# Kernel tuning notes

Measured on AMD Instinct MI355X. Metric: run time of the kernel, lower is better.

## Reference

```python
import jax, jax.numpy as jnp
import numpy as np

B, N, IN, HD, NH, L, OUT = 256, 128, 9, 128, 8, 4, 60
DH = HD // NH
ALPHA = 0.6
EPS = 1e-5

def _ln(x, g, b):
    m = jnp.mean(x, axis=-1, keepdims=True)
    v = jnp.mean((x - m) ** 2, axis=-1, keepdims=True)
    return (x - m) * jax.lax.rsqrt(v + EPS) * g + b

def setup_inputs():
    key = jax.random.key(0)
    ks = jax.random.split(key, 30)
    p = lambda i, s: jax.random.normal(ks[i], s, jnp.float32) * 0.02
    strong = (jax.random.uniform(ks[25], (N, N)) < 0.15).astype(jnp.float32)
    strong = jnp.maximum(strong, jnp.eye(N, dtype=jnp.float32))  # self loops
    weak_mask = (jax.random.uniform(ks[26], (N, N)) < 0.10).astype(jnp.float32)
    return {
        'x': jax.random.normal(ks[0], (B, N, IN), jnp.float32),
        'conv_w': p(1, (HD, IN)), 'conv_b': p(2, (HD,)),
        'bn_gamma': jnp.ones((HD,), jnp.float32), 'bn_beta': jnp.zeros((HD,), jnp.float32),
        'bn_mean': jnp.zeros((HD,), jnp.float32), 'bn_var': jnp.ones((HD,), jnp.float32),
        'W': p(3, (L, HD, HD)), 'a_src': p(4, (L, NH, DH)), 'a_dst': p(5, (L, NH, DH)),
        'ln_g': jnp.ones((L, HD), jnp.float32), 'ln_b': jnp.zeros((L, HD), jnp.float32),
        'ffn_w1': p(6, (L, HD, 2 * HD)), 'ffn_b1': p(7, (L, 2 * HD)),
        'ffn_w2': p(8, (L, 2 * HD, HD)), 'ffn_b2': p(9, (L, HD)),
        'norm_g': jnp.ones((HD,), jnp.float32), 'norm_b': jnp.zeros((HD,), jnp.float32),
        'proj_w': p(10, (HD, HD)), 'proj_b': p(11, (HD,)),
        'head_w1': p(12, (HD, HD // 2)), 'head_b1': p(13, (HD // 2,)),
        'head_w2': p(14, (HD // 2, OUT)), 'head_b2': p(15, (OUT,)),
        'strong_adj': strong, 'weak_mask': weak_mask,
        'weak_param': p(16, (N, N)), 'edge_weight_adj': p(17, (N, N)),
    }

def reference(x, conv_w, conv_b, bn_gamma, bn_beta, bn_mean, bn_var, W, a_src, a_dst, ln_g, ln_b, ffn_w1, ffn_b1, ffn_w2, ffn_b2, norm_g, norm_b, proj_w, proj_b, head_w1, head_b1, head_w2, head_b2, strong_adj, weak_mask, weak_param, edge_weight_adj):
    # embedding: Conv1d(k=1) == per-node linear, then eval-mode BatchNorm1d + ReLU
    h = jnp.einsum('bni,oi->bno', x, conv_w) + conv_b  # [B,N,HD]
    h = (h - bn_mean) * jax.lax.rsqrt(bn_var + EPS) * bn_gamma + bn_beta
    h = jax.nn.relu(h)
    # weak adjacency: learnable gated edges, row-normalized (shared across layers)
    Aw = jax.nn.sigmoid(weak_param) * weak_mask
    Aw = Aw / (jnp.sum(Aw, axis=-1, keepdims=True) + EPS)  # [N,N]
    for i in range(L):
        res = h
        hp = jnp.einsum('bnd,de->bne', h, W[i]).reshape(B, N, NH, DH)
        s = jnp.einsum('bnhd,hd->bnh', hp, a_src[i])
        t = jnp.einsum('bnhd,hd->bnh', hp, a_dst[i])
        e = jax.nn.leaky_relu(s[:, :, None, :] + t[:, None, :, :], 0.2)  # [B,N,N,H]
        e = e + edge_weight_adj[None, :, :, None]  # learned per-edge bias
        e = jnp.where(strong_adj[None, :, :, None] > 0, e, jnp.float32(-1e9))
        att = jax.nn.softmax(e, axis=2)  # softmax over neighbors j
        strong_out = jnp.einsum('bijh,bjhd->bihd', att, hp)
        weak_out = jnp.einsum('ij,bjhd->bihd', Aw, hp)
        g = jax.nn.relu(ALPHA * strong_out + (1.0 - ALPHA) * weak_out).reshape(B, N, HD)
        g = _ln(g, ln_g[i], ln_b[i])
        g = jax.nn.relu(g @ ffn_w1[i] + ffn_b1[i]) @ ffn_w2[i] + ffn_b2[i]
        h = g + res
    h = _ln(h, norm_g, norm_b)
    h = h @ proj_w + proj_b
    h = jnp.mean(h, axis=1)  # mean-pool over nodes -> [B,HD]
    h = jax.nn.relu(h @ head_w1 + head_b1)
    return h @ head_w2 + head_b2  # [B,OUT]
```

## Files before the change

kernel.cpp:

```cpp
#include <hip/hip_runtime.h>
#include <hip/hip_bf16.h>

typedef __hip_bfloat16 bf16;
typedef unsigned short u16;
typedef __attribute__((ext_vector_type(8))) short bfrag;
typedef __attribute__((ext_vector_type(4))) float cfrag;

union BF { bfrag v; u16 u[8]; unsigned w[4]; };
union CF { cfrag v; float f[4]; };

#define MFMA(a,b,c) __builtin_amdgcn_mfma_f32_16x16x32_bf16(a,b,c,0,0,0)

#define BB   256
#define NN   128
#define IND  9
#define HDD  128
#define LLY  4
#define OUTD 60
#define LOG2E 1.44269504f
#define STR  136

__device__ __forceinline__ float b2f(bf16 v){ return __bfloat162float(v); }
__device__ __forceinline__ float u2f(u16 u){ return __uint_as_float(((unsigned)u) << 16); }
__device__ __forceinline__ u16 f2bf_bits(float f){
    unsigned u = __float_as_uint(f);
    return (u16)((u + 0x7FFFu + ((u >> 16) & 1u)) >> 16);
}
__device__ __forceinline__ unsigned pk2(float a, float b){
    union { __hip_bfloat162 h; unsigned u; } c;
    c.h = __float22bfloat162_rn(make_float2(a, b));
    return c.u;
}
__device__ __forceinline__ float wave_sum(float v){
    #pragma unroll
    for (int m = 32; m; m >>= 1) v += __shfl_xor(v, m, 64);
    return v;
}
__device__ __forceinline__ float ldin(const void* p, int i, bool isbf){
    return isbf ? b2f(((const bf16*)p)[i]) : ((const float*)p)[i];
}

struct SrcPtrs { const void* p[28]; };

__device__ const int NCV_OFF[19] = {0,1152,1280,1408,1536,1664,1792,2304,2816,3840,
                                    4352,4480,4608,20992,21120,29312,29376,33216,33276};
__device__ const int NCV_SRC[18] = {1,2,3,4,5,6,10,11,13,15,16,17,18,19,20,21,22,23};

__global__ __launch_bounds__(256) void k_prep(
    SrcPtrs S, float* __restrict__ pf,
    u16* __restrict__ WT, u16* __restrict__ w1T, u16* __restrict__ w2T,
    u16* __restrict__ WAb, u16* __restrict__ ew2, u16* __restrict__ Aw16,
    int* __restrict__ flagOut)
{
    const unsigned* xw = (const unsigned*)S.p[0];
    int lane = threadIdx.x & 63;
    int cnt = 0;
    for (int i = lane; i < 512; i += 64) {
        float v = __uint_as_float((xw[i] & 0xFFFFu) << 16);
        if (!(fabsf(v) < 32.f)) cnt++;
    }
    bool isbf = wave_sum((float)cnt) < 16.f;
    if (blockIdx.x == 0 && threadIdx.x == 0) *flagOut = isbf ? 1 : 0;

    int blk = blockIdx.x, tid = threadIdx.x;
    if (blk < 131) {
        int idx = blk * 256 + tid;
        if (idx < 33276) {
            int y = 17;
            #pragma unroll 1
            for (int t = 1; t < 18; t++) if (idx < NCV_OFF[t]) { y = t - 1; break; }
            pf[idx] = ldin(S.p[NCV_SRC[y]], idx - NCV_OFF[y], isbf);
        }
    } else if (blk < 387) {
        int j = (blk - 131) * 256 + tid;
        int l = j >> 14, r = j & 16383, n = r >> 7, k = r & 127;
        WT[j] = f2bf_bits(ldin(S.p[7], (l << 14) + k * 128 + n, isbf));
    } else if (blk < 899) {
        int j = (blk - 387) * 256 + tid;
        int l = j >> 15, r = j & 32767, n = r >> 7, k = r & 127;
        w1T[j] = f2bf_bits(ldin(S.p[12], (l << 15) + k * 256 + n, isbf));
    } else if (blk < 1411) {
        int j = (blk - 899) * 256 + tid;
        int l = j >> 15, r = j & 32767, n = r >> 8, k = r & 255;
        w2T[j] = f2bf_bits(ldin(S.p[14], (l << 15) + k * 128 + n, isbf));
    } else if (blk < 1443) {
        int j = (blk - 1411) * 256 + tid;
        int l = j >> 11, r = j & 2047, n = r >> 7, k = r & 127;
        int h = n & 7;
        const void* ap = (n < 8) ? S.p[8] : S.p[9];
        float sacc = 0.f;
        #pragma unroll 1
        for (int d = 0; d < 16; d++)
            sacc += ldin(S.p[7], l * 16384 + k * 128 + h * 16 + d, isbf)
                  * ldin(ap, l * 128 + h * 16 + d, isbf);
        WAb[j] = f2bf_bits(sacc);
    } else if (blk < 1507) {
        int j = (blk - 1443) * 256 + tid;
        float sav = ldin(S.p[24], j, isbf);
        float ewv = ldin(S.p[27], j, isbf);
        ew2[j] = f2bf_bits(sav > 0.f ? ewv * LOG2E : -1e30f);
    } else {
        __shared__ float red[2];
        int i = blk - 1507, j = tid & 127;
        float v = 0.f;
        if (tid < 128) {
            float wmv = ldin(S.p[25], i * 128 + j, isbf);
            float wpv = ldin(S.p[26], i * 128 + j, isbf);
            v = wmv / (1.f + __expf(-wpv));
            float sm = wave_sum(v);
            if ((tid & 63) == 0) red[tid >> 6] = sm;
        }
        __syncthreads();
        if (tid < 128) {
            float tot = red[0] + red[1];
            Aw16[i * 128 + j] = f2bf_bits(v / (tot + 1e-5f));
        }
    }
}

#define LDSB (2*128*STR*2 + 8192)
__global__ __launch_bounds__(512, 2) void k_net(
    const void* __restrict__ xraw, const int* __restrict__ flag,
    const float* __restrict__ pf,
    const u16* __restrict__ WTg, const u16* __restrict__ WAbg,
    const u16* __restrict__ Awg, const u16* __restrict__ ew2g,
    const u16* __restrict__ w1Tg, const u16* __restrict__ w2Tg,
    void* __restrict__ outv)
{
    extern __shared__ __align__(16) char smem[];
    u16* Abuf = (u16*)smem;
    u16* Bbuf = Abuf + 128 * STR;
    float* st2 = (float*)(Bbuf + 128 * STR);
    float* s2  = st2;
    u16*   t2u = (u16*)(st2 + 1024);

    const int b = blockIdx.x;
    const int tid = threadIdx.x, lane = tid & 63, wv = tid >> 6;
    const int l15 = lane & 15, kg = lane >> 4;
    const int wrow = wv * 16;
    const bool isbf = (*flag != 0);

    float hreg[8][4];

    {
        float xr[4][9];
        #pragma unroll
        for (int r = 0; r < 4; r++) {
            int bn = b * NN + wrow + kg * 4 + r;
            #pragma unroll
            for (int k = 0; k < IND; k++) xr[r][k] = ldin(xraw, bn * IND + k, isbf);
        }
        #pragma unroll 1
        for (int nt = 0; nt < 8; nt++) {
            int d = nt * 16 + l15;
            float cwreg[IND];
            #pragma unroll
            for (int k = 0; k < IND; k++) cwreg[k] = pf[d * IND + k];
            float scale = rsqrtf(pf[1664 + d] + 1e-5f) * pf[1280 + d];
            float bias  = pf[1408 + d] - pf[1536 + d] * scale;
            float cbd   = pf[1152 + d];
            #pragma unroll
            for (int r = 0; r < 4; r++) {
                float a = cbd;
                #pragma unroll
                for (int k = 0; k < IND; k++) a = fmaf(xr[r][k], cwreg[k], a);
                a = fmaxf(fmaf(a, scale, bias), 0.f);
                hreg[nt][r] = a;
                Abuf[(wrow + kg * 4 + r) * STR + d] = f2bf_bits(a);
            }
        }
    }

    const int arow = wrow + l15;

    #pragma unroll 1
    for (int l = 0; l < LLY; l++) {
        const u16* WT  = WTg  + l * 16384;
        const u16* WAb = WAbg + l * 2048;
        const u16* w1T = w1Tg + l * 32768;
        const u16* w2T = w2Tg + l * 32768;
        const float* fb1 = pf + 2816 + l * 256;
        const float* fb2 = pf + 3840 + l * 128;
        const float* lng = pf + 1792 + l * 128;
        const float* lnb = pf + 2304 + l * 128;

        __syncthreads();

        {
            CF acc[8], ast;
            #pragma unroll
            for (int r = 0; r < 4; r++) ast.f[r] = 0.f;
            #pragma unroll
            for (int nt = 0; nt < 8; nt++)
                #pragma unroll
                for (int r = 0; r < 4; r++) acc[nt].f[r] = 0.f;
            #pragma unroll 1
            for (int kk = 0; kk < 4; kk++) {
                bfrag af  = *(const bfrag*)&Abuf[arow * STR + kk*32 + kg*8];
                bfrag wab = *(const bfrag*)&WAb[l15 * 128 + kk*32 + kg*8];
                ast.v = MFMA(af, wab, ast.v);
                #pragma unroll
                for (int nt = 0; nt < 8; nt++) {
                    bfrag bw = *(const bfrag*)&WT[(nt*16 + l15) * 128 + kk*32 + kg*8];
                    acc[nt].v = MFMA(af, bw, acc[nt].v);
                }
            }
            #pragma unroll
            for (int nt = 0; nt < 8; nt++) {
                int col = nt*16 + l15;
                #pragma unroll
                for (int rp = 0; rp < 2; rp++) {
                    int row = wrow + kg*4 + rp*2;
                    *(unsigned*)&Bbuf[col * STR + row] = pk2(acc[nt].f[rp*2], acc[nt].f[rp*2+1]);
                }
            }
            #pragma unroll
            for (int r = 0; r < 4; r++) {
                int node = wrow + kg*4 + r;
                float v = ast.f[r] * LOG2E;
                if (l15 < 8) s2[l15 * 128 + node] = v;
                else         t2u[(l15 - 8) * 128 + node] = f2bf_bits(v);
            }
        }
        __syncthreads();

        CF accW[8];
        #pragma unroll
        for (int nt = 0; nt < 8; nt++)
            #pragma unroll
            for (int r = 0; r < 4; r++) accW[nt].f[r] = 0.f;
        #pragma unroll 1
        for (int kk = 0; kk < 4; kk++) {
            bfrag awf = *(const bfrag*)&Awg[arow * 128 + kk*32 + kg*8];
            #pragma unroll
            for (int nt = 0; nt < 8; nt++) {
                bfrag hb2 = *(const bfrag*)&Bbuf[(nt*16 + l15) * STR + kk*32 + kg*8];
                accW[nt].v = MFMA(awf, hb2, accW[nt].v);
            }
        }

        CF accS[8];
        #pragma unroll
        for (int nt = 0; nt < 8; nt++)
            #pragma unroll
            for (int r = 0; r < 4; r++) accS[nt].f[r] = 0.f;
        #pragma unroll 1
        for (int h = 0; h < 8; h++) {
            bfrag hb[4];
            #pragma unroll
            for (int kk = 0; kk < 4; kk++)
                hb[kk] = *(const bfrag*)&Bbuf[(h*16 + l15) * STR + kk*32 + kg*8];
            float sA = s2[h * 128 + arow];
            float pv[4][8];
            float sm = 0.f;
            #pragma unroll
            for (int kk = 0; kk < 4; kk++) {
                BF tb; tb.v = *(const bfrag*)&t2u[h * 128 + kk*32 + kg*8];
                BF e2; e2.v = *(const bfrag*)&ew2g[arow * 128 + kk*32 + kg*8];
                #pragma unroll
                for (int j = 0; j < 8; j++) {
                    float x2 = sA + u2f(tb.u[j]);
                    float lk = fmaxf(x2, 0.2f * x2);
                    float p = __builtin_amdgcn_exp2f(lk + u2f(e2.u[j]));
                    pv[kk][j] = p; sm += p;
                }
            }
            sm += __shfl_xor(sm, 16, 64);
            sm += __shfl_xor(sm, 32, 64);
            float inv = __builtin_amdgcn_rcpf(sm);
            #pragma unroll
            for (int kk = 0; kk < 4; kk++) {
                BF pb;
                #pragma unroll
                for (int q = 0; q < 4; q++)
                    pb.w[q] = pk2(pv[kk][2*q] * inv, pv[kk][2*q+1] * inv);
                accS[h].v = MFMA(pb.v, hb[kk], accS[h].v);
            }
        }
        __syncthreads();

        {
            float gv[8][4];
            #pragma unroll
            for (int nt = 0; nt < 8; nt++)
                #pragma unroll
                for (int r = 0; r < 4; r++)
                    gv[nt][r] = fmaxf(0.6f * accS[nt].f[r] + 0.4f * accW[nt].f[r], 0.f);
            #pragma unroll
            for (int r = 0; r < 4; r++) {
                float s1 = 0.f, sq = 0.f;
                #pragma unroll
                for (int nt = 0; nt < 8; nt++) { float x = gv[nt][r]; s1 += x; sq = fmaf(x, x, sq); }
                #pragma unroll
                for (int m = 1; m <= 8; m <<= 1) { s1 += __shfl_xor(s1, m, 64); sq += __shfl_xor(sq, m, 64); }
                float mu = s1 * (1.f / 128.f);
                float var = sq * (1.f / 128.f) - mu * mu;
                float rs = rsqrtf(fmaxf(var, 0.f) + 1e-5f);
                #pragma unroll
                for (int nt = 0; nt < 8; nt++) {
                    int col = nt*16 + l15;
                    Bbuf[(wrow + kg*4 + r) * STR + col] =
                        f2bf_bits(fmaf((gv[nt][r] - mu) * rs, lng[col], lnb[col]));
                }
            }
        }

        CF acc2[8];
        #pragma unroll
        for (int nt = 0; nt < 8; nt++)
            #pragma unroll
            for (int r = 0; r < 4; r++) acc2[nt].f[r] = 0.f;
        #pragma unroll 1
        for (int nh = 0; nh < 2; nh++) {
            CF a1[8];
            #pragma unroll
            for (int nt = 0; nt < 8; nt++)
                #pragma unroll
                for (int r = 0; r < 4; r++) a1[nt].f[r] = 0.f;
            #pragma unroll 1
            for (int kk = 0; kk < 4; kk++) {
                bfrag gf = *(const bfrag*)&Bbuf[arow * STR + kk*32 + kg*8];
                #pragma unroll
                for (int nt = 0; nt < 8; nt++) {
                    bfrag wf = *(const bfrag*)&w1T[(nh*128 + nt*16 + l15) * 128 + kk*32 + kg*8];
                    a1[nt].v = MFMA(gf, wf, a1[nt].v);
                }
            }
            #pragma unroll
            for (int nt = 0; nt < 8; nt++) {
                int col = nt*16 + l15;
                float b1v = fb1[nh*128 + col];
                #pragma unroll
                for (int r = 0; r < 4; r++)
                    Abuf[(wrow + kg*4 + r) * STR + col] = f2bf_bits(fmaxf(a1[nt].f[r] + b1v, 0.f));
            }
            #pragma unroll 1
            for (int kk = 0; kk < 4; kk++) {
                bfrag hf = *(const bfrag*)&Abuf[arow * STR + kk*32 + kg*8];
                #pragma unroll
                for (int nt = 0; nt < 8; nt++) {
                    bfrag wf = *(const bfrag*)&w2T[(nt*16 + l15) * 256 + nh*128 + kk*32 + kg*8];
                    acc2[nt].v = MFMA(hf, wf, acc2[nt].v);
                }
            }
        }

        #pragma unroll
        for (int nt = 0; nt < 8; nt++) {
            float b2v = fb2[nt*16 + l15];
            #pragma unroll
            for (int r = 0; r < 4; r++) hreg[nt][r] += acc2[nt].f[r] + b2v;
        }
        if (l < LLY - 1) {
            #pragma unroll
            for (int nt = 0; nt < 8; nt++) {
                int col = nt*16 + l15;
                #pragma unroll
                for (int r = 0; r < 4; r++)
                    Abuf[(wrow + kg*4 + r) * STR + col] = f2bf_bits(hreg[nt][r]);
            }
        }
    }

    const float* ng = pf + 4352;
    const float* nb = pf + 4480;
    float pacc[8];
    #pragma unroll
    for (int nt = 0; nt < 8; nt++) pacc[nt] = 0.f;
    #pragma unroll
    for (int r = 0; r < 4; r++) {
        float s1 = 0.f, sq = 0.f;
        #pragma unroll
        for (int nt = 0; nt < 8; nt++) { float x = hreg[nt][r]; s1 += x; sq = fmaf(x, x, sq); }
        #pragma unroll
        for (int m = 1; m <= 8; m <<= 1) { s1 += __shfl_xor(s1, m, 64); sq += __shfl_xor(sq, m, 64); }
        float mu = s1 * (1.f / 128.f);
        float var = sq * (1.f / 128.f) - mu * mu;
        float rs = rsqrtf(fmaxf(var, 0.f) + 1e-5f);
        #pragma unroll
        for (int nt = 0; nt < 8; nt++) {
            int col = nt*16 + l15;
            pacc[nt] += fmaf((hreg[nt][r] - mu) * rs, ng[col], nb[col]);
        }
    }
    #pragma unroll
    for (int nt = 0; nt < 8; nt++) {
        pacc[nt] += __shfl_xor(pacc[nt], 16, 64);
        pacc[nt] += __shfl_xor(pacc[nt], 32, 64);
    }
    __syncthreads();
    if (kg == 0) {
        #pragma unroll
        for (int nt = 0; nt < 8; nt++) st2[wv * 128 + nt*16 + l15] = pacc[nt];
    }
    __syncthreads();
    if (tid < 128) {
        float tot = 0.f;
        #pragma unroll
        for (int w = 0; w < 8; w++) tot += st2[w * 128 + tid];
        st2[1024 + tid] = tot * (1.f / 128.f);
    }
    __syncthreads();
    {
        int e = tid & 127, kq = tid >> 7;
        float a = 0.f;
        #pragma unroll 4
        for (int k = kq * 32; k < kq * 32 + 32; k++)
            a = fmaf(st2[1024 + k], pf[4608 + k * 128 + e], a);
        st2[1152 + kq * 128 + e] = a;
    }
    __syncthreads();
    if (tid < 128)
        st2[1664 + tid] = st2[1152 + tid] + st2[1280 + tid] + st2[1408 + tid] + st2[1536 + tid]
                        + pf[20992 + tid];
    __syncthreads();
    if (tid < 64) {
        float a1 = pf[29312 + tid];
        #pragma unroll 4
        for (int k = 0; k < 128; k++) a1 = fmaf(st2[1664 + k], pf[21120 + k * 64 + tid], a1);
        st2[1792 + tid] = fmaxf(a1, 0.f);
    }
    __syncthreads();
    if (tid < OUTD) {
        float a2 = pf[33216 + tid];
        #pragma unroll 4
        for (int k = 0; k < 64; k++) a2 = fmaf(st2[1792 + k], pf[29376 + k * OUTD + tid], a2);
        if (isbf) ((bf16*)outv)[b * OUTD + tid] = __float2bfloat16(a2);
        else      ((float*)outv)[b * OUTD + tid] = a2;
    }
}

extern "C" void kernel_launch(void* const* d_in, const int* in_sizes, int n_in,
                              void* d_out, int out_size, void* d_ws, size_t ws_size,
                              hipStream_t stream)
{
    float* ws = (float*)d_ws;
    float* pf = ws;
    int*   flag = (int*)(ws + 33280);
    u16* WT16   = (u16*)(ws + 33536);
    u16* w1T16  = WT16 + 65536;
    u16* w2T16  = w1T16 + 131072;
    u16* WAb16  = w2T16 + 131072;
    u16* Aw16   = WAb16 + 8192;
    u16* ew2p   = Aw16 + 16384;

    SrcPtrs S;
    for (int i = 0; i < 28; i++) S.p[i] = d_in[i];

    hipFuncSetAttribute((const void*)k_net,
                        hipFuncAttributeMaxDynamicSharedMemorySize, LDSB);

    k_prep<<<1635, 256, 0, stream>>>(S, pf, WT16, w1T16, w2T16, WAb16, ew2p, Aw16, flag);
    k_net<<<BB, 512, LDSB, stream>>>(d_in[0], flag, pf,
                                     WT16, WAb16, Aw16, ew2p, w1T16, w2T16, d_out);
}
```

Measured before the change: 352.9 us.

## Tile weight transposes in prep and fold weak aggregation into attention accumulator

The prep kernel now transposes weights through a shared-memory tile, which gives coalesced reads and shrinks the grid from 1635 to 435 blocks. In the main kernel, the residual state moves from registers into an fp32 LDS buffer to free registers. Softmax normalisation is deferred: unnormalised probabilities feed the MFMA and are scaled per row afterwards. The weak-adjacency matmul, with 0.4 folded into Aw, accumulates into the same accumulators, and several k-loops are fully unrolled. LDS use grows by about 68KB, which may reduce occupancy below the 2 blocks per CU the launch bounds request.

Result: slower. 401.5 us (+13.8%).

```diff
diff --git a/kernel.cpp b/kernel.cpp
--- a/kernel.cpp
+++ b/kernel.cpp
@@ -52,6 +52,7 @@
     u16* __restrict__ WAb, u16* __restrict__ ew2, u16* __restrict__ Aw16,
     int* __restrict__ flagOut)
 {
+    __shared__ float tile[64][65];
     const unsigned* xw = (const unsigned*)S.p[0];
     int lane = threadIdx.x & 63;
     int cnt = 0;
@@ -71,20 +72,35 @@
             for (int t = 1; t < 18; t++) if (idx < NCV_OFF[t]) { y = t - 1; break; }
             pf[idx] = ldin(S.p[NCV_SRC[y]], idx - NCV_OFF[y], isbf);
         }
-    } else if (blk < 387) {
-        int j = (blk - 131) * 256 + tid;
-        int l = j >> 14, r = j & 16383, n = r >> 7, k = r & 127;
-        WT[j] = f2bf_bits(ldin(S.p[7], (l << 14) + k * 128 + n, isbf));
-    } else if (blk < 899) {
-        int j = (blk - 387) * 256 + tid;
-        int l = j >> 15, r = j & 32767, n = r >> 7, k = r & 127;
-        w1T[j] = f2bf_bits(ldin(S.p[12], (l << 15) + k * 256 + n, isbf));
-    } else if (blk < 1411) {
-        int j = (blk - 899) * 256 + tid;
-        int l = j >> 15, r = j & 32767, n = r >> 8, k = r & 255;
-        w2T[j] = f2bf_bits(ldin(S.p[14], (l << 15) + k * 128 + n, isbf));
-    } else if (blk < 1443) {
-        int j = (blk - 1411) * 256 + tid;
+    } else if (blk < 211) {
+        const void* src; u16* dst; int K, N, k0, n0;
+        if (blk < 147) {
+            int t = blk - 131, l = t >> 2, tt = t & 3;
+            src = (const char*)S.p[7] + (size_t)l * 16384 * (isbf ? 2 : 4);
+            dst = WT + l * 16384; K = 128; N = 128; k0 = (tt >> 1) * 64; n0 = (tt & 1) * 64;
+        } else if (blk < 179) {
+            int t = blk - 147, l = t >> 3, tt = t & 7;
+            src = (const char*)S.p[12] + (size_t)l * 32768 * (isbf ? 2 : 4);
+            dst = w1T + l * 32768; K = 128; N = 256; k0 = (tt >> 2) * 64; n0 = (tt & 3) * 64;
+        } else {
+            int t = blk - 179, l = t >> 3, tt = t & 7;
+            src = (const char*)S.p[14] + (size_t)l * 32768 * (isbf ? 2 : 4);
+            dst = w2T + l * 32768; K = 256; N = 128; k0 = (tt & 3) * 64; n0 = (tt >> 2) * 64;
+        }
+        int ty = tid >> 6, tx = tid & 63;
+        #pragma unroll 4
+        for (int i = 0; i < 16; i++) {
+            int row = ty * 16 + i;
+            tile[row][tx] = ldin(src, (k0 + row) * N + n0 + tx, isbf);
+        }
+        __syncthreads();
+        #pragma unroll 4
+        for (int i = 0; i < 16; i++) {
+            int row = ty * 16 + i;
+            dst[(n0 + row) * K + k0 + tx] = f2bf_bits(tile[tx][row]);
+        }
+    } else if (blk < 243) {
+        int j = (blk - 211) * 256 + tid;
         int l = j >> 11, r = j & 2047, n = r >> 7, k = r & 127;
         int h = n & 7;
         const void* ap = (n < 8) ? S.p[8] : S.p[9];
@@ -94,14 +110,14 @@
             sacc += ldin(S.p[7], l * 16384 + k * 128 + h * 16 + d, isbf)
                   * ldin(ap, l * 128 + h * 16 + d, isbf);
         WAb[j] = f2bf_bits(sacc);
-    } else if (blk < 1507) {
-        int j = (blk - 1443) * 256 + tid;
+    } else if (blk < 307) {
+        int j = (blk - 243) * 256 + tid;
         float sav = ldin(S.p[24], j, isbf);
         float ewv = ldin(S.p[27], j, isbf);
         ew2[j] = f2bf_bits(sav > 0.f ? ewv * LOG2E : -1e30f);
     } else {
         __shared__ float red[2];
-        int i = blk - 1507, j = tid & 127;
+        int i = blk - 307, j = tid & 127;
         float v = 0.f;
         if (tid < 128) {
             float wmv = ldin(S.p[25], i * 128 + j, isbf);
@@ -113,12 +129,12 @@
         __syncthreads();
         if (tid < 128) {
             float tot = red[0] + red[1];
-            Aw16[i * 128 + j] = f2bf_bits(v / (tot + 1e-5f));
-        }
-    }
-}
-
-#define LDSB (2*128*STR*2 + 8192)
+            Aw16[i * 128 + j] = f2bf_bits(0.4f * v / (tot + 1e-5f));
+        }
+    }
+}
+
+#define LDSB (128*STR*2*2 + 128*132*4 + 2560*4)
 __global__ __launch_bounds__(512, 2) void k_net(
     const void* __restrict__ xraw, const int* __restrict__ flag,
     const float* __restrict__ pf,
@@ -128,22 +144,23 @@
     void* __restrict__ outv)
 {
     extern __shared__ __align__(16) char smem[];
-    u16* Abuf = (u16*)smem;
-    u16* Bbuf = Abuf + 128 * STR;
-    float* st2 = (float*)(Bbuf + 128 * STR);
-    float* s2  = st2;
-    u16*   t2u = (u16*)(st2 + 1024);
+    u16* U1 = (u16*)smem;
+    u16* U2 = U1 + 128 * STR;
+    float* hf32 = (float*)(U2 + 128 * STR);
+    float* st2  = hf32 + 128 * 132;
+    float* s2   = st2;
+    u16*   t2u  = (u16*)(st2 + 1024);
+    float* invb = st2 + 1536;
 
     const int b = blockIdx.x;
     const int tid = threadIdx.x, lane = tid & 63, wv = tid >> 6;
     const int l15 = lane & 15, kg = lane >> 4;
     const int wrow = wv * 16;
+    const int arow = wrow + l15;
     const bool isbf = (*flag != 0);
 
-    float hreg[8][4];
-
     {
-        float xr[4][9];
+        float xr[4][IND];
         #pragma unroll
         for (int r = 0; r < 4; r++) {
             int bn = b * NN + wrow + kg * 4 + r;
@@ -165,13 +182,12 @@
                 #pragma unroll
                 for (int k = 0; k < IND; k++) a = fmaf(xr[r][k], cwreg[k], a);
                 a = fmaxf(fmaf(a, scale, bias), 0.f);
-                hreg[nt][r] = a;
-                Abuf[(wrow + kg * 4 + r) * STR + d] = f2bf_bits(a);
-            }
-        }
-    }
-
-    const int arow = wrow + l15;
+                int row = wrow + kg * 4 + r;
+                hf32[row * 132 + d] = a;
+                U1[row * STR + d] = f2bf_bits(a);
+            }
+        }
+    }
 
     #pragma unroll 1
     for (int l = 0; l < LLY; l++) {
@@ -194,9 +210,9 @@
             for (int nt = 0; nt < 8; nt++)
                 #pragma unroll
                 for (int r = 0; r < 4; r++) acc[nt].f[r] = 0.f;
-            #pragma unroll 1
+            #pragma unroll
             for (int kk = 0; kk < 4; kk++) {
-                bfrag af  = *(const bfrag*)&Abuf[arow * STR + kk*32 + kg*8];
+                bfrag af  = *(const bfrag*)&U1[arow * STR + kk*32 + kg*8];
                 bfrag wab = *(const bfrag*)&WAb[l15 * 128 + kk*32 + kg*8];
                 ast.v = MFMA(af, wab, ast.v);
                 #pragma unroll
@@ -211,7 +227,7 @@
                 #pragma unroll
                 for (int rp = 0; rp < 2; rp++) {
                     int row = wrow + kg*4 + rp*2;
-                    *(unsigned*)&Bbuf[col * STR + row] = pk2(acc[nt].f[rp*2], acc[nt].f[rp*2+1]);
+                    *(unsigned*)&U2[col * STR + row] = pk2(acc[nt].f[rp*2], acc[nt].f[rp*2+1]);
                 }
             }
             #pragma unroll
@@ -224,87 +240,79 @@
         }
         __syncthreads();
 
-        CF accW[8];
+        CF accS[8];
         #pragma unroll
         for (int nt = 0; nt < 8; nt++)
             #pragma unroll
-            for (int r = 0; r < 4; r++) accW[nt].f[r] = 0.f;
-        #pragma unroll 1
-        for (int kk = 0; kk < 4; kk++) {
-            bfrag awf = *(const bfrag*)&Awg[arow * 128 + kk*32 + kg*8];
-            #pragma unroll
-            for (int nt = 0; nt < 8; nt++) {
-                bfrag hb2 = *(const bfrag*)&Bbuf[(nt*16 + l15) * STR + kk*32 + kg*8];
-                accW[nt].v = MFMA(awf, hb2, accW[nt].v);
-            }
-        }
-
-        CF accS[8];
-        #pragma unroll
-        for (int nt = 0; nt < 8; nt++)
-            #pragma unroll
             for (int r = 0; r < 4; r++) accS[nt].f[r] = 0.f;
+        BF e2f[4];
+        #pragma unroll
+        for (int kk = 0; kk < 4; kk++)
+            e2f[kk].v = *(const bfrag*)&ew2g[arow * 128 + kk*32 + kg*8];
         #pragma unroll 1
         for (int h = 0; h < 8; h++) {
-            bfrag hb[4];
-            #pragma unroll
-            for (int kk = 0; kk < 4; kk++)
-                hb[kk] = *(const bfrag*)&Bbuf[(h*16 + l15) * STR + kk*32 + kg*8];
             float sA = s2[h * 128 + arow];
-            float pv[4][8];
             float sm = 0.f;
             #pragma unroll
             for (int kk = 0; kk < 4; kk++) {
+                bfrag hb = *(const bfrag*)&U2[(h*16 + l15) * STR + kk*32 + kg*8];
                 BF tb; tb.v = *(const bfrag*)&t2u[h * 128 + kk*32 + kg*8];
-                BF e2; e2.v = *(const bfrag*)&ew2g[arow * 128 + kk*32 + kg*8];
+                BF pb;
+                float p0[8];
                 #pragma unroll
                 for (int j = 0; j < 8; j++) {
                     float x2 = sA + u2f(tb.u[j]);
                     float lk = fmaxf(x2, 0.2f * x2);
-                    float p = __builtin_amdgcn_exp2f(lk + u2f(e2.u[j]));
-                    pv[kk][j] = p; sm += p;
+                    float p = __builtin_amdgcn_exp2f(lk + u2f(e2f[kk].u[j]));
+                    p0[j] = p; sm += p;
                 }
+                #pragma unroll
+                for (int q = 0; q < 4; q++) pb.w[q] = pk2(p0[2*q], p0[2*q+1]);
+                accS[h].v = MFMA(pb.v, hb, accS[h].v);
             }
             sm += __shfl_xor(sm, 16, 64);
             sm += __shfl_xor(sm, 32, 64);
-            float inv = __builtin_amdgcn_rcpf(sm);
-            #pragma unroll
-            for (int kk = 0; kk < 4; kk++) {
-                BF pb;
-                #pragma unroll
-                for (int q = 0; q < 4; q++)
-                    pb.w[q] = pk2(pv[kk][2*q] * inv, pv[kk][2*q+1] * inv);
-                accS[h].v = MFMA(pb.v, hb[kk], accS[h].v);
-            }
-        }
+            invb[h * 128 + arow] = 0.6f * __builtin_amdgcn_rcpf(sm);
+        }
+        #pragma unroll
+        for (int h = 0; h < 8; h++) {
+            const float4 iv = *(const float4*)&invb[h * 128 + wrow + kg*4];
+            accS[h].f[0] *= iv.x; accS[h].f[1] *= iv.y;
+            accS[h].f[2] *= iv.z; accS[h].f[3] *= iv.w;
+        }
+
+        #pragma unroll
+        for (int kk = 0; kk < 4; kk++) {
+            bfrag awf = *(const bfrag*)&Awg[arow * 128 + kk*32 + kg*8];
+            #pragma unroll
+            for (int nt = 0; nt < 8; nt++) {
+                bfrag hb2 = *(const bfrag*)&U2[(nt*16 + l15) * STR + kk*32 + kg*8];
+                accS[nt].v = MFMA(awf, hb2, accS[nt].v);
+            }
+        }
+
+        #pragma unroll
+        for (int r = 0; r < 4; r++) {
+            float s1 = 0.f, sq = 0.f;
+            #pragma unroll
+            for (int nt = 0; nt < 8; nt++) {
+                float x = fmaxf(accS[nt].f[r], 0.f);
+                accS[nt].f[r] = x; s1 += x; sq = fmaf(x, x, sq);
+            }
+            #pragma unroll
+            for (int m = 1; m <= 8; m <<= 1) { s1 += __shfl_xor(s1, m, 64); sq += __shfl_xor(sq, m, 64); }
+            float mu = s1 * (1.f / 128.f);
+            float var = sq * (1.f / 128.f) - mu * mu;
+            float rs = rsqrtf(fmaxf(var, 0.f) + 1e-5f);
+            #pragma unroll
+            for (int nt = 0; nt < 8; nt++) {
+                int col = nt*16 + l15;
+                U1[(wrow + kg*4 + r) * STR + col] =
+                    f2bf_bits(fmaf((accS[nt].f[r] - mu) * rs, lng[col], lnb[col]));
+            }
+        }
+
         __syncthreads();
-
-        {
-            float gv[8][4];
-            #pragma unroll
-            for (int nt = 0; nt < 8; nt++)
-                #pragma unroll
-                for (int r = 0; r < 4; r++)
-                    gv[nt][r] = fmaxf(0.6f * accS[nt].f[r] + 0.4f * accW[nt].f[r], 0.f);
-            #pragma unroll
-            for (int r = 0; r < 4; r++) {
-                float s1 = 0.f, sq = 0.f;
-                #pragma unroll
-                for (int nt = 0; nt < 8; nt++) { float x = gv[nt][r]; s1 += x; sq = fmaf(x, x, sq); }
-                #pragma unroll
-                for (int m = 1; m <= 8; m <<= 1) { s1 += __shfl_xor(s1, m, 64); sq += __shfl_xor(sq, m, 64); }
-                float mu = s1 * (1.f / 128.f);
-                float var = sq * (1.f / 128.f) - mu * mu;
-                float rs = rsqrtf(fmaxf(var, 0.f) + 1e-5f);
-                #pragma unroll
-                for (int nt = 0; nt < 8; nt++) {
-                    int col = nt*16 + l15;
-                    Bbuf[(wrow + kg*4 + r) * STR + col] =
-                        f2bf_bits(fmaf((gv[nt][r] - mu) * rs, lng[col], lnb[col]));
-                }
-            }
-        }
-
         CF acc2[8];
         #pragma unroll
         for (int nt = 0; nt < 8; nt++)
@@ -317,9 +325,9 @@
             for (int nt = 0; nt < 8; nt++)
                 #pragma unroll
                 for (int r = 0; r < 4; r++) a1[nt].f[r] = 0.f;
-            #pragma unroll 1
+            #pragma unroll
             for (int kk = 0; kk < 4; kk++) {
-                bfrag gf = *(const bfrag*)&Bbuf[arow * STR + kk*32 + kg*8];
+                bfrag gf = *(const bfrag*)&U1[arow * STR + kk*32 + kg*8];
                 #pragma unroll
                 for (int nt = 0; nt < 8; nt++) {
                     bfrag wf = *(const bfrag*)&w1T[(nh*128 + nt*16 + l15) * 128 + kk*32 + kg*8];
@@ -332,11 +340,11 @@
                 float b1v = fb1[nh*128 + col];
                 #pragma unroll
                 for (int r = 0; r < 4; r++)
-                    Abuf[(wrow + kg*4 + r) * STR + col] = f2bf_bits(fmaxf(a1[nt].f[r] + b1v, 0.f));
-            }
-            #pragma unroll 1
+                    U2[(wrow + kg*4 + r) * STR + col] = f2bf_bits(fmaxf(a1[nt].f[r] + b1v, 0.f));
+            }
+            #pragma unroll
             for (int kk = 0; kk < 4; kk++) {
-                bfrag hf = *(const bfrag*)&Abuf[arow * STR + kk*32 + kg*8];
+                bfrag hf = *(const bfrag*)&U2[arow * STR + kk*32 + kg*8];
                 #pragma unroll
                 for (int nt = 0; nt < 8; nt++) {
                     bfrag wf = *(const bfrag*)&w2T[(nt*16 + l15) * 256 + nh*128 + kk*32 + kg*8];
@@ -347,17 +355,14 @@
 
         #pragma unroll
         for (int nt = 0; nt < 8; nt++) {
-            float b2v = fb2[nt*16 + l15];
-            #pragma unroll
-            for (int r = 0; r < 4; r++) hreg[nt][r] += acc2[nt].f[r] + b2v;
-        }
-        if (l < LLY - 1) {
-            #pragma unroll
-            for (int nt = 0; nt < 8; nt++) {
-                int col = nt*16 + l15;
-                #pragma unroll
-                for (int r = 0; r < 4; r++)
-                    Abuf[(wrow + kg*4 + r) * STR + col] = f2bf_bits(hreg[nt][r]);
+            int col = nt*16 + l15;
+            float b2v = fb2[col];
+            #pragma unroll
+            for (int r = 0; r < 4; r++) {
+                int row = wrow + kg*4 + r;
+                float hv = hf32[row * 132 + col] + acc2[nt].f[r] + b2v;
+                hf32[row * 132 + col] = hv;
+                if (l < LLY - 1) U1[row * STR + col] = f2bf_bits(hv);
             }
         }
     }
@@ -369,19 +374,22 @@
     for (int nt = 0; nt < 8; nt++) pacc[nt] = 0.f;
     #pragma unroll
     for (int r = 0; r < 4; r++) {
+        int row = wrow + kg*4 + r;
+        float hvv[8];
         float s1 = 0.f, sq = 0.f;
         #pragma unroll
-        for (int nt = 0; nt < 8; nt++) { float x = hreg[nt][r]; s1 += x; sq = fmaf(x, x, sq); }
+        for (int nt = 0; nt < 8; nt++) {
+            float x = hf32[row * 132 + nt*16 + l15];
+            hvv[nt] = x; s1 += x; sq = fmaf(x, x, sq);
+        }
         #pragma unroll
         for (int m = 1; m <= 8; m <<= 1) { s1 += __shfl_xor(s1, m, 64); sq += __shfl_xor(sq, m, 64); }
         float mu = s1 * (1.f / 128.f);
         float var = sq * (1.f / 128.f) - mu * mu;
         float rs = rsqrtf(fmaxf(var, 0.f) + 1e-5f);
         #pragma unroll
-        for (int nt = 0; nt < 8; nt++) {
-            int col = nt*16 + l15;
-            pacc[nt] += fmaf((hreg[nt][r] - mu) * rs, ng[col], nb[col]);
-        }
+        for (int nt = 0; nt < 8; nt++)
+            pacc[nt] += fmaf((hvv[nt] - mu) * rs, ng[nt*16 + l15], nb[nt*16 + l15]);
     }
     #pragma unroll
     for (int nt = 0; nt < 8; nt++) {
@@ -450,7 +458,7 @@
     hipFuncSetAttribute((const void*)k_net,
                         hipFuncAttributeMaxDynamicSharedMemorySize, LDSB);
 
-    k_prep<<<1635, 256, 0, stream>>>(S, pf, WT16, w1T16, w2T16, WAb16, ew2p, Aw16, flag);
+    k_prep<<<435, 256, 0, stream>>>(S, pf, WT16, w1T16, w2T16, WAb16, ew2p, Aw16, flag);
     k_net<<<BB, 512, LDSB, stream>>>(d_in[0], flag, pf,
                                      WT16, WAb16, Aw16, ew2p, w1T16, w2T16, d_out);
 }
```
